# Kernel tuning notes

Hardware: AMD Instinct MI355X
Metric: run time of the kernel (lower is better)

The kernel has to match this reference:

```python
import jax, jax.numpy as jnp
import numpy as np

GROUPS = 32
EPS = 1e-5


def setup_inputs() -> dict:
    key = jax.random.key(0)
    ks = jax.random.split(key, 4)
    B, C, H, W = 32, 512, 32, 32
    x = jax.random.normal(ks[0], (B, C, H, W), dtype=jnp.float32)
    gn_gamma = jnp.ones((C,), jnp.float32)
    gn_beta = jnp.zeros((C,), jnp.float32)
    qkv_w = jax.random.normal(ks[1], (3 * C, C), dtype=jnp.float32) * 0.02
    qkv_b = jnp.zeros((3 * C,), jnp.float32)
    proj_w = jax.random.normal(ks[2], (C, C), dtype=jnp.float32) * 0.02
    proj_b = jnp.zeros((C,), jnp.float32)
    return {"x": x, "gn_gamma": gn_gamma, "gn_beta": gn_beta,
            "qkv_w": qkv_w, "qkv_b": qkv_b, "proj_w": proj_w, "proj_b": proj_b}


def group_norm(x, gamma, beta):
    B, C, H, W = x.shape
    xr = x.reshape(B, GROUPS, C // GROUPS, H, W)
    mean = xr.mean(axis=(2, 3, 4), keepdims=True)
    var = xr.var(axis=(2, 3, 4), keepdims=True)
    xn = ((xr - mean) * jax.lax.rsqrt(var + EPS)).reshape(B, C, H, W)
    return xn * gamma[None, :, None, None] + beta[None, :, None, None]


def reference(x, gn_gamma, gn_beta, qkv_w, qkv_b, proj_w, proj_b):
    B, C, H, W = x.shape
    h_in = group_norm(x, gn_gamma, gn_beta)
    # 1x1 conv == per-pixel matmul over channels
    qkv = jnp.einsum('oc,bchw->bohw', qkv_w, h_in) + qkv_b[None, :, None, None]
    q, k, v = jnp.split(qkv, 3, axis=1)
    scale = 1.0 / jnp.sqrt(jnp.sqrt(jnp.float32(C)))  # 1/sqrt(sqrt(C)), applied to q and k
    attn = jnp.einsum('bchw,bcij->bhwij', q * scale, k * scale)  # [B,H,W,H,W]
    attn = jax.nn.softmax(attn, axis=-1)  # faithful: softmax over last axis (j) only
    h = jnp.einsum('bhwij,bcij->bchw', attn, v)
    h = jnp.einsum('oc,bchw->bohw', proj_w, h) + proj_b[None, :, None, None]
    return x + h
```

## Files before the change

kernel.cpp:

```cpp
#include <hip/hip_runtime.h>

typedef __attribute__((ext_vector_type(8))) short short8;
typedef __attribute__((ext_vector_type(4))) float f32x4;

__device__ __forceinline__ float b2f(unsigned short u) {
  union { unsigned u32; float f; } x; x.u32 = ((unsigned)u) << 16; return x.f;
}
__device__ __forceinline__ unsigned short f2bf(float f) {
  union { float f; unsigned u; } x; x.f = f;
  unsigned r = x.u + 0x7fffu + ((x.u >> 16) & 1u);
  return (unsigned short)(r >> 16);
}
__device__ __forceinline__ void async_load16(const void* g, void* l) {
  __builtin_amdgcn_global_load_lds(
      (__attribute__((address_space(1))) void*)(void*)(g),
      (__attribute__((address_space(3))) void*)(l), 16, 0, 0);
}

__global__ __launch_bounds__(256) void prep_k(
    const float* __restrict__ x, const float* __restrict__ gamma,
    const float* __restrict__ beta, unsigned short* __restrict__ hin,
    const float* __restrict__ wa, unsigned short* __restrict__ oa,
    const float* __restrict__ wb, unsigned short* __restrict__ ob) {
  if (blockIdx.x >= 1024) {
    int i = (blockIdx.x - 1024) * 256 + threadIdx.x;
    const float* src; unsigned short* dst; int idx;
    if (i < 196608) { src = wa; dst = oa; idx = i; }
    else if (i < 262144) { src = wb; dst = ob; idx = i - 196608; }
    else return;
    float4 v = ((const float4*)src)[idx];
    unsigned short o[4] __attribute__((aligned(8)));
    o[0] = f2bf(v.x); o[1] = f2bf(v.y); o[2] = f2bf(v.z); o[3] = f2bf(v.w);
    ((int2*)dst)[idx] = *(int2*)o;
    return;
  }
  const int b = blockIdx.x >> 5, g = blockIdx.x & 31;
  const float* xb = x + ((unsigned long long)b * 512ull + (unsigned long long)g * 16ull) * 1024ull;
  const int t = threadIdx.x;
  float4 xr[16];
  float s = 0.f, ss = 0.f;
#pragma unroll
  for (int c = 0; c < 16; ++c) {
    xr[c] = *(const float4*)(xb + c * 1024 + t * 4);
    s += xr[c].x + xr[c].y + xr[c].z + xr[c].w;
    ss += xr[c].x * xr[c].x + xr[c].y * xr[c].y + xr[c].z * xr[c].z + xr[c].w * xr[c].w;
  }
#pragma unroll
  for (int o = 32; o; o >>= 1) { s += __shfl_down(s, o); ss += __shfl_down(ss, o); }
  __shared__ float sred[8];
  if ((t & 63) == 0) { sred[t >> 6] = s; sred[4 + (t >> 6)] = ss; }
  __syncthreads();
  s = sred[0] + sred[1] + sred[2] + sred[3];
  ss = sred[4] + sred[5] + sred[6] + sred[7];
  const float mean = s * (1.f / 16384.f);
  const float rstd = rsqrtf(ss * (1.f / 16384.f) - mean * mean + 1e-5f);
  float ga[16], be[16];
#pragma unroll
  for (int c = 0; c < 16; ++c) {
    float gg = gamma[g * 16 + c] * rstd;
    ga[c] = gg;
    be[c] = beta[g * 16 + c] - mean * gg;
  }
#pragma unroll
  for (int p4 = 0; p4 < 4; ++p4) {
    unsigned short ov[16] __attribute__((aligned(16)));
#pragma unroll
    for (int c = 0; c < 16; ++c)
      ov[c] = f2bf(((const float*)&xr[c])[p4] * ga[c] + be[c]);
    unsigned short* dst = hin + ((unsigned long long)b * 1024ull + t * 4 + p4) * 512ull + g * 16;
    *(int4*)dst = *(int4*)ov;
    *(int4*)(dst + 8) = *(int4*)(ov + 8);
  }
}

template <int MODE, int MI>
__global__ __launch_bounds__(256, 4) void gemm_k(
    const unsigned short* __restrict__ A, unsigned long long sA, int lda,
    const unsigned short* __restrict__ B, unsigned long long sB, int ldb,
    const float* __restrict__ bias, const float* __restrict__ xres,
    unsigned short* __restrict__ out0, unsigned short* __restrict__ out1,
    unsigned short* __restrict__ out2, float* __restrict__ fout,
    float scale, int K) {
  constexpr int MBLK = MI * 32;
  constexpr int STAGE_SHORTS = MBLK * 64 + 128 * 64;
  constexpr int SMEM_SHORTS = (MODE == 3) ? (128 * 66 * 2) : STAGE_SHORTS;
  __shared__ unsigned short smem[SMEM_SHORTS];
  unsigned short* As = smem;
  unsigned short* Bs = smem + MBLK * 64;
  const int tid = threadIdx.x;
  const int wave = tid >> 6, lane = tid & 63;

  int n_t, m_t, b;
  if (MODE == 0) {
    const int L = blockIdx.x + gridDim.x * (blockIdx.y + gridDim.y * blockIdx.z);
    const int r8 = L & 7, q = L >> 3;
    n_t = q % 12;
    const int mb = (q / 12) * 8 + r8;
    m_t = mb & 7;
    b = mb >> 3;
  } else if (MODE == 1) {
    const int L = blockIdx.x + gridDim.x * (blockIdx.y + gridDim.y * blockIdx.z);
    const int slice = L & 7, t = L >> 3;
    b = slice * 4 + (t >> 6);
    const int rem = t & 63;
    m_t = rem >> 3;
    n_t = rem & 7;
  } else if (MODE == 2) {
    const int L = blockIdx.x + gridDim.x * (blockIdx.y + gridDim.y * blockIdx.z);
    const int slice = L & 7, t = L >> 3;
    b = slice * 4 + (t >> 5);
    const int rem = t & 31;
    m_t = rem >> 2;
    n_t = rem & 3;
  } else {
    n_t = blockIdx.x; m_t = blockIdx.y; b = blockIdx.z;
  }
  const int m0 = m_t * MBLK, n0 = n_t * 128;
  const int wm = (wave & 1) * (MI * 16), wn = (wave >> 1) * 64;
  const unsigned short* Ab = A + (unsigned long long)b * sA + (unsigned long long)m0 * lda;
  const unsigned short* Bb = B + (unsigned long long)b * sB + (unsigned long long)n0 * ldb;

  f32x4 acc[MI][4];
#pragma unroll
  for (int i = 0; i < MI; ++i)
#pragma unroll
    for (int j = 0; j < 4; ++j)
#pragma unroll
      for (int r = 0; r < 4; ++r) acc[i][j][r] = 0.f;

  const int lrow = lane & 15;
  const int lk = lane >> 4;
  const int sr = lane >> 3;
  const int pc = (((lane & 7) ^ sr) << 3);
  const int r7 = lrow & 7;

  for (int kt = 0; kt < K; kt += 64) {
    {
#pragma unroll
      for (int c = 0; c < MBLK / 32; ++c) {
        const int row = wave * (MBLK / 4) + c * 8;
        async_load16(Ab + kt + (unsigned long long)(row + sr) * lda + pc,
                     (void*)(As + row * 64));
      }
#pragma unroll
      for (int c = 0; c < 4; ++c) {
        const int row = wave * 32 + c * 8;
        async_load16(Bb + kt + (unsigned long long)(row + sr) * ldb + pc,
                     (void*)(Bs + row * 64));
      }
    }
    __syncthreads();
#pragma unroll
    for (int ks = 0; ks < 2; ++ks) {
      const int ko = (((ks << 2) + lk) ^ r7) << 3;
      short8 af[MI], bfr[4];
#pragma unroll
      for (int i = 0; i < MI; ++i)
        af[i] = *(const short8*)(As + (wm + i * 16 + lrow) * 64 + ko);
#pragma unroll
      for (int i = 0; i < 4; ++i)
        bfr[i] = *(const short8*)(Bs + (wn + i * 16 + lrow) * 64 + ko);
#pragma unroll
      for (int mi = 0; mi < MI; ++mi)
#pragma unroll
        for (int ni = 0; ni < 4; ++ni)
          acc[mi][ni] = __builtin_amdgcn_mfma_f32_16x16x32_bf16(af[mi], bfr[ni], acc[mi][ni], 0, 0, 0);
    }
    __syncthreads();
  }

  const int r0 = lk * 4;
  const int cn = lrow;

  if (MODE == 0) {
    const int which = n0 >> 9;
#pragma unroll
    for (int ni = 0; ni < 4; ++ni) {
      const int o = n0 + wn + ni * 16 + cn;
      const float bi = bias[o];
      const int oin = o & 511;
      if (which < 2) {
        unsigned short* dst = (which == 0 ? out0 : out1) + (unsigned long long)b * 524288ull;
#pragma unroll
        for (int mi = 0; mi < MI; ++mi) {
          const int pbase = m0 + wm + mi * 16 + r0;
#pragma unroll
          for (int r = 0; r < 4; ++r)
            dst[(unsigned long long)(pbase + r) * 512ull + oin] = f2bf((acc[mi][ni][r] + bi) * scale);
        }
      } else {
        unsigned short* dst = out2 + (unsigned long long)b * 524288ull + (unsigned long long)oin * 1024ull;
#pragma unroll
        for (int mi = 0; mi < MI; ++mi) {
          const int pbase = m0 + wm + mi * 16 + r0;
          unsigned short h4[4] __attribute__((aligned(8)));
#pragma unroll
          for (int r = 0; r < 4; ++r) h4[r] = f2bf(acc[mi][ni][r] + bi);
          *(int2*)(dst + pbase) = *(int2*)h4;
        }
      }
    }
  } else if (MODE == 1) {
#pragma unroll
    for (int mi = 0; mi < MI; ++mi)
#pragma unroll
      for (int ni = 0; ni < 4; ++ni)
#pragma unroll
        for (int r = 0; r < 4; ++r) acc[mi][ni][r] = __expf(acc[mi][ni][r]);
    float inv[4][MI / 2];
#pragma unroll
    for (int ni = 0; ni < 4; ++ni)
#pragma unroll
      for (int cp = 0; cp < MI / 2; ++cp) {
        float s8 = 0.f;
#pragma unroll
        for (int mm = 0; mm < 2; ++mm)
#pragma unroll
          for (int r = 0; r < 4; ++r) s8 += acc[cp * 2 + mm][ni][r];
        s8 += __shfl_xor(s8, 16);
        s8 += __shfl_xor(s8, 32);
        inv[ni][cp] = 1.f / s8;
      }
    unsigned short* Pt = smem;
    unsigned short* dst = out0 + (unsigned long long)b * 1048576ull;
#pragma unroll
    for (int half = 0; half < 2; ++half) {
      __syncthreads();
      if ((wn >> 6) == half) {
#pragma unroll
        for (int mi = 0; mi < MI; ++mi)
#pragma unroll
          for (int ni = 0; ni < 4; ++ni) {
            unsigned short p4[4] __attribute__((aligned(8)));
#pragma unroll
            for (int r = 0; r < 4; ++r) p4[r] = f2bf(acc[mi][ni][r] * inv[ni][mi >> 1]);
            const int li = ni * 16 + cn;
            const int lj = wm + mi * 16 + r0;
            *(int2*)(Pt + li * 136 + lj) = *(int2*)p4;
          }
      }
      __syncthreads();
#pragma unroll
      for (int it = 0; it < 4; ++it) {
        const int row = it * 16 + (tid >> 4);
        const int col = (tid & 15) * 8;
        int4 v = *(const int4*)(Pt + row * 136 + col);
        *(int4*)(dst + (unsigned long long)(n0 + half * 64 + row) * 1024ull + m0 + col) = v;
      }
    }
  } else if (MODE == 2) {
    unsigned short* dst = out0 + (unsigned long long)b * 524288ull;
#pragma unroll
    for (int mi = 0; mi < MI; ++mi) {
      const int ib = m0 + wm + mi * 16 + r0;
#pragma unroll
      for (int ni = 0; ni < 4; ++ni) {
        const int c = n0 + wn + ni * 16 + cn;
#pragma unroll
        for (int r = 0; r < 4; ++r)
          dst[(unsigned long long)(ib + r) * 512ull + c] = f2bf(acc[mi][ni][r]);
      }
    }
  } else {
    float* Pt = (float*)smem;
    float* dst = fout + (unsigned long long)b * 524288ull;
    const float* xr = xres + (unsigned long long)b * 524288ull;
#pragma unroll
    for (int half = 0; half < 2; ++half) {
      __syncthreads();
      if ((wn >> 6) == half) {
#pragma unroll
        for (int mi = 0; mi < MI; ++mi)
#pragma unroll
          for (int ni = 0; ni < 4; ++ni) {
            const int col = ni * 16 + cn;
#pragma unroll
            for (int r = 0; r < 4; ++r)
              Pt[(wm + mi * 16 + r0 + r) * 66 + col] = acc[mi][ni][r];
          }
      }
      __syncthreads();
#pragma unroll
      for (int it = 0; it < 8; ++it) {
        const int row = it * 16 + (tid >> 4);
        const int col = (tid & 15) * 4;
        const int o = m0 + row;
        const unsigned long long gidx = (unsigned long long)o * 1024ull + n0 + half * 64 + col;
        const float* ps = Pt + row * 66 + col;
        const float bi = bias[o];
        const float4 xv = *(const float4*)(xr + gidx);
        float4 ov;
        ov.x = ps[0] + bi + xv.x;
        ov.y = ps[1] + bi + xv.y;
        ov.z = ps[2] + bi + xv.z;
        ov.w = ps[3] + bi + xv.w;
        *(float4*)(dst + gidx) = ov;
      }
    }
  }
}

extern "C" void kernel_launch(void* const* d_in, const int* in_sizes, int n_in,
                              void* d_out, int out_size, void* d_ws, size_t ws_size,
                              hipStream_t stream) {
  const float* x     = (const float*)d_in[0];
  const float* gamma = (const float*)d_in[1];
  const float* beta  = (const float*)d_in[2];
  const float* qkvw  = (const float*)d_in[3];
  const float* qkvb  = (const float*)d_in[4];
  const float* projw = (const float*)d_in[5];
  const float* projb = (const float*)d_in[6];
  float* out = (float*)d_out;
  char* ws = (char*)d_ws;

  unsigned short* Hin = (unsigned short*)(ws);
  unsigned short* Q   = (unsigned short*)(ws + 1ull * 33554432ull);
  unsigned short* Kb  = (unsigned short*)(ws + 2ull * 33554432ull);
  unsigned short* V   = (unsigned short*)(ws + 3ull * 33554432ull);
  unsigned short* S   = (unsigned short*)(ws + 4ull * 33554432ull);
  unsigned short* Wq  = (unsigned short*)(ws + 6ull * 33554432ull);
  unsigned short* Wp  = (unsigned short*)(ws + 6ull * 33554432ull + 2ull * 1048576ull);
  unsigned short* H   = Hin;

  const float SCALE = 0.21022410381342864f;
  dim3 blk(256);
  const float* nzf = nullptr;
  unsigned short* nzo = nullptr;
  float* nzfo = nullptr;

  hipLaunchKernelGGL(prep_k, dim3(2048), blk, 0, stream,
                     x, gamma, beta, Hin, qkvw, Wq, projw, Wp);
  hipLaunchKernelGGL((gemm_k<0, 4>), dim3(3072), blk, 0, stream,
                     Hin, 524288ull, 512, Wq, 0ull, 512, qkvb, nzf, Q, Kb, V, nzfo, SCALE, 512);
  hipLaunchKernelGGL((gemm_k<1, 4>), dim3(2048), blk, 0, stream,
                     Kb, 524288ull, 512, Q, 524288ull, 512, nzf, nzf, S, nzo, nzo, nzfo, 0.f, 512);
  hipLaunchKernelGGL((gemm_k<2, 4>), dim3(1024), blk, 0, stream,
                     S, 1048576ull, 1024, V, 524288ull, 1024, nzf, nzf, H, nzo, nzo, nzfo, 0.f, 1024);
  hipLaunchKernelGGL((gemm_k<3, 4>), dim3(8, 4, 32), blk, 0, stream,
                     Wp, 0ull, 512, H, 524288ull, 512, projb, x, nzo, nzo, nzo, out, 0.f, 512);
}
```

Before: 313.0 us.

## Double-buffer GEMM LDS tiles with async prefetch two K-steps ahead

Splits the GEMM shared-memory tile into two buffers and issues async global-to-LDS loads for the next K-tiles while the current tile is being consumed by MFMAs. Partial vmcnt waits and raw s_barrier replace the full __syncthreads pair, so memory latency can overlap with compute. It also relaxes launch bounds from 4 to 2 blocks per CU, giving each thread more registers. The costs are double the LDS per block and possibly lower occupancy. The hard-coded vmcnt(8) is only correct when each thread issues exactly eight loads per stage, i.e. MI=4.

```diff
diff --git a/kernel.cpp b/kernel.cpp
--- a/kernel.cpp
+++ b/kernel.cpp
@@ -74,7 +74,7 @@
 }
 
 template <int MODE, int MI>
-__global__ __launch_bounds__(256, 4) void gemm_k(
+__global__ __launch_bounds__(256, 2) void gemm_k(
     const unsigned short* __restrict__ A, unsigned long long sA, int lda,
     const unsigned short* __restrict__ B, unsigned long long sB, int ldb,
     const float* __restrict__ bias, const float* __restrict__ xres,
@@ -82,11 +82,8 @@
     unsigned short* __restrict__ out2, float* __restrict__ fout,
     float scale, int K) {
   constexpr int MBLK = MI * 32;
-  constexpr int STAGE_SHORTS = MBLK * 64 + 128 * 64;
-  constexpr int SMEM_SHORTS = (MODE == 3) ? (128 * 66 * 2) : STAGE_SHORTS;
-  __shared__ unsigned short smem[SMEM_SHORTS];
-  unsigned short* As = smem;
-  unsigned short* Bs = smem + MBLK * 64;
+  constexpr int BUF_SHORTS = MBLK * 64 + 128 * 64;
+  __shared__ unsigned short smem[2 * BUF_SHORTS];
   const int tid = threadIdx.x;
   const int wave = tid >> 6, lane = tid & 63;
 
@@ -134,22 +131,35 @@
   const int pc = (((lane & 7) ^ sr) << 3);
   const int r7 = lrow & 7;
 
-  for (int kt = 0; kt < K; kt += 64) {
-    {
-#pragma unroll
-      for (int c = 0; c < MBLK / 32; ++c) {
-        const int row = wave * (MBLK / 4) + c * 8;
-        async_load16(Ab + kt + (unsigned long long)(row + sr) * lda + pc,
-                     (void*)(As + row * 64));
-      }
-#pragma unroll
-      for (int c = 0; c < 4; ++c) {
-        const int row = wave * 32 + c * 8;
-        async_load16(Bb + kt + (unsigned long long)(row + sr) * ldb + pc,
-                     (void*)(Bs + row * 64));
-      }
-    }
-    __syncthreads();
+  auto STAGE = [&](int kt, int buf) {
+    unsigned short* As_ = smem + buf * BUF_SHORTS;
+    unsigned short* Bs_ = As_ + MBLK * 64;
+#pragma unroll
+    for (int c = 0; c < MBLK / 32; ++c) {
+      const int row = wave * (MBLK / 4) + c * 8;
+      async_load16(Ab + kt + (unsigned long long)(row + sr) * lda + pc,
+                   (void*)(As_ + row * 64));
+    }
+#pragma unroll
+    for (int c = 0; c < 4; ++c) {
+      const int row = wave * 32 + c * 8;
+      async_load16(Bb + kt + (unsigned long long)(row + sr) * ldb + pc,
+                   (void*)(Bs_ + row * 64));
+    }
+  };
+
+  const int nt = K >> 6;
+  STAGE(0, 0);
+  STAGE(64, 1);
+  for (int t = 0; t < nt; ++t) {
+    if (t + 1 < nt) {
+      asm volatile("s_waitcnt vmcnt(8)" ::: "memory");
+    } else {
+      asm volatile("s_waitcnt vmcnt(0)" ::: "memory");
+    }
+    __builtin_amdgcn_s_barrier();
+    const unsigned short* As = smem + (t & 1) * BUF_SHORTS;
+    const unsigned short* Bs = As + MBLK * 64;
 #pragma unroll
     for (int ks = 0; ks < 2; ++ks) {
       const int ko = (((ks << 2) + lk) ^ r7) << 3;
@@ -166,7 +176,10 @@
         for (int ni = 0; ni < 4; ++ni)
           acc[mi][ni] = __builtin_amdgcn_mfma_f32_16x16x32_bf16(af[mi], bfr[ni], acc[mi][ni], 0, 0, 0);
     }
-    __syncthreads();
+    if (t + 2 < nt) {
+      __builtin_amdgcn_s_barrier();
+      STAGE((t + 2) << 6, t & 1);
+    }
   }
 
   const int r0 = lk * 4;
```

After: 323.9 us. +3.5%, slower.
